# Performance work log

Hardware: AMD Instinct MI355X
Metric: run time of the kernel (lower is better)

The kernel has to match this reference:

```python
import jax, jax.numpy as jnp
import numpy as np

NUM_USERS = 40000
NUM_BUSINESSES = 60000
N = NUM_USERS + NUM_BUSINESSES
HIDDEN = 128
HEADS = 4
E = 200000
BATCH = 4096
NEG_SLOPE = 0.2  # PyG GATConv default


def setup_inputs() -> dict:
    key = jax.random.key(0)
    ks = jax.random.split(key, 20)
    s = 0.05
    inp = {
        "user_table": jax.random.normal(ks[0], (NUM_USERS, HIDDEN), jnp.float32) * s,
        "business_table": jax.random.normal(ks[1], (NUM_BUSINESSES, HIDDEN), jnp.float32) * s,
        # gat1: in=HIDDEN, out=HIDDEN, heads=HEADS
        "W1": jax.random.normal(ks[2], (HIDDEN, HEADS * HIDDEN), jnp.float32) * s,
        "att_src1": jax.random.normal(ks[3], (HEADS, HIDDEN), jnp.float32) * s,
        "att_dst1": jax.random.normal(ks[4], (HEADS, HIDDEN), jnp.float32) * s,
        "b1": jnp.zeros((HEADS * HIDDEN,), jnp.float32),
        # gat2: in=HEADS*HIDDEN, out=HIDDEN, heads=1
        "W2": jax.random.normal(ks[5], (HEADS * HIDDEN, HIDDEN), jnp.float32) * s,
        "att_src2": jax.random.normal(ks[6], (1, HIDDEN), jnp.float32) * s,
        "att_dst2": jax.random.normal(ks[7], (1, HIDDEN), jnp.float32) * s,
        "b2": jnp.zeros((HIDDEN,), jnp.float32),
        # predictor MLP
        "Wp1": jax.random.normal(ks[8], (2 * HIDDEN, HIDDEN), jnp.float32) * s,
        "bp1": jnp.zeros((HIDDEN,), jnp.float32),
        "Wp2": jax.random.normal(ks[9], (HIDDEN, 1), jnp.float32) * s,
        "bp2": jnp.zeros((1,), jnp.float32),
        "user_idx": jax.random.randint(ks[10], (BATCH,), 0, NUM_USERS),
        "business_idx": jax.random.randint(ks[11], (BATCH,), 0, NUM_BUSINESSES) + NUM_USERS,
        "edge_index": jax.random.randint(ks[12], (2, E), 0, N),
    }
    return inp


def gat_conv(x, edge_index, W, att_src, att_dst, bias, heads, out_ch, num_nodes):
    # add self-loops (PyG default add_self_loops=True)
    loop = jnp.arange(num_nodes)
    src = jnp.concatenate([edge_index[0], loop])
    dst = jnp.concatenate([edge_index[1], loop])
    h = (x @ W).reshape(num_nodes, heads, out_ch)            # [N,H,C]
    a_src = jnp.einsum('nhc,hc->nh', h, att_src)             # [N,H]
    a_dst = jnp.einsum('nhc,hc->nh', h, att_dst)             # [N,H]
    e = jax.nn.leaky_relu(a_src[src] + a_dst[dst], NEG_SLOPE)  # [E',H]
    # segment softmax over destination nodes
    emax = jax.ops.segment_max(e, dst, num_segments=num_nodes)
    emax = jnp.where(jnp.isfinite(emax), emax, 0.0)
    ex = jnp.exp(e - emax[dst])
    denom = jax.ops.segment_sum(ex, dst, num_segments=num_nodes)
    alpha = ex / (denom[dst] + 1e-16)                        # [E',H]
    msg = h[src] * alpha[..., None]                          # [E',H,C]
    out = jax.ops.segment_sum(msg, dst, num_segments=num_nodes)  # [N,H,C]
    return out.reshape(num_nodes, heads * out_ch) + bias


def reference(user_table, business_table, W1, att_src1, att_dst1, b1,
              W2, att_src2, att_dst2, b2, Wp1, bp1, Wp2, bp2,
              user_idx, business_idx, edge_index):
    user_emb = user_table[user_idx]                          # [B,HIDDEN]
    business_emb = business_table[business_idx - NUM_USERS]  # [B,HIDDEN]
    x = jnp.zeros((N, HIDDEN), jnp.float32)
    x = x.at[user_idx].set(user_emb)
    x = x.at[business_idx].set(business_emb)
    x = jax.nn.relu(gat_conv(x, edge_index, W1, att_src1, att_dst1, b1, HEADS, HIDDEN, N))
    x = gat_conv(x, edge_index, W2, att_src2, att_dst2, b2, 1, HIDDEN, N)
    feats = jnp.concatenate([x[user_idx], x[business_idx]], axis=1)  # [B,2*HIDDEN]
    hidden = jax.nn.relu(feats @ Wp1 + bp1)
    rating = hidden @ Wp2 + bp2                              # [B,1]
    return rating.squeeze(-1)
```

## Files before the change

kernel.cpp:

```cpp
#include <hip/hip_runtime.h>
#include <cstdint>
#include <cstddef>

#define NU      40000
#define NBZ     60000
#define NN      100000
#define HID     128
#define NHEADS  4
#define NE      200000
#define NBATCH  4096
#define BE      (2 * NBATCH)
#define SMAX    10240
#define CAP     16
#define SLOPE   0.2f

typedef __attribute__((ext_vector_type(8))) short short8v;
typedef __attribute__((ext_vector_type(4))) float f32x4;

__device__ __forceinline__ float lrelu(float x) { return x > 0.f ? x : SLOPE * x; }
__device__ __forceinline__ unsigned short f2bf(float f) {
  unsigned u = __float_as_uint(f);
  u += 0x7FFFu + ((u >> 16) & 1u);
  return (unsigned short)(u >> 16);
}

__global__ void k_init(int* __restrict__ node2slotB, int* __restrict__ flags,
                       int* __restrict__ cnt,
                       const float* __restrict__ W1, const float* __restrict__ W2,
                       const float* __restrict__ Wp1,
                       short* __restrict__ w1t, short* __restrict__ w2t,
                       short* __restrict__ wp1t) {
  int i = blockIdx.x * blockDim.x + threadIdx.x;
  if (i < NN) { node2slotB[i] = -1; flags[i] = 0; }
  if (i < NHEADS * HID * HID) {
    int c = i >> 14, nk = i & 16383, n = nk >> 7, k = nk & 127;
    w1t[i] = (short)f2bf(W1[(size_t)k * 512 + c * 128 + n]);
    w2t[i] = (short)f2bf(W2[(size_t)(c * 128 + k) * 128 + n]);
  }
  if (i < HID * 256) {
    int n = i >> 8, k = i & 255;
    wp1t[i] = (short)f2bf(Wp1[(size_t)k * HID + n]);
  }
  if (i == 0) *cnt = 0;
}

__global__ void k_mark(const int* __restrict__ user_idx, const int* __restrict__ business_idx,
                       int* __restrict__ node2slotB) {
  int i = blockIdx.x * blockDim.x + threadIdx.x;
  if (i >= BE) return;
  int node = (i < NBATCH) ? user_idx[i] : business_idx[i - NBATCH];
  node2slotB[node] = i;
}

#define W1ATT_BLOCKS 64
__global__ __launch_bounds__(256)
void k_frontA(const float* __restrict__ W1,
              const float* __restrict__ att_src1, const float* __restrict__ att_dst1,
              float* __restrict__ wsrc, float* __restrict__ wdst,
              const int* __restrict__ ei, const int* __restrict__ n2sB,
              int* __restrict__ flags) {
  int bid = blockIdx.x, tid = threadIdx.x;
  if (bid >= W1ATT_BLOCKS) {
    int e = (bid - W1ATT_BLOCKS) * 256 + tid;
    if (e < NE) {
      int s = ei[e], d = ei[NE + e];
      if (n2sB[d] >= 0) atomicOr(&flags[s], 2);
      if (n2sB[s] >= 0) atomicOr(&flags[d], 1);
    }
    return;
  }
  __shared__ float red[2][2][8];
  int kk = tid >> 7, c = tid & 127;
  int k = bid * 2 + kk;
  float ps[4], pd[4];
#pragma unroll
  for (int h = 0; h < 4; ++h) {
    float wv = W1[(size_t)k * 512 + h * 128 + c];
    ps[h] = wv * att_src1[h * 128 + c];
    pd[h] = wv * att_dst1[h * 128 + c];
  }
#pragma unroll
  for (int off = 1; off < 64; off <<= 1) {
#pragma unroll
    for (int h = 0; h < 4; ++h) { ps[h] += __shfl_xor(ps[h], off); pd[h] += __shfl_xor(pd[h], off); }
  }
  int half = (tid >> 6) & 1;
  if ((tid & 63) == 0) {
#pragma unroll
    for (int h = 0; h < 4; ++h) { red[kk][half][h] = ps[h]; red[kk][half][h + 4] = pd[h]; }
  }
  __syncthreads();
  if ((tid & 127) == 0) {
#pragma unroll
    for (int h = 0; h < 4; ++h) {
      wsrc[k * 4 + h] = red[kk][0][h] + red[kk][1][h];
      wdst[k * 4 + h] = red[kk][0][h + 4] + red[kk][1][h + 4];
    }
  }
}

#define SCAL1_BLOCKS (BE / 4)
__global__ __launch_bounds__(256)
void k_mid(const float* __restrict__ user_table, const float* __restrict__ business_table,
           const int* __restrict__ user_idx, const int* __restrict__ business_idx,
           const float* __restrict__ wsrc, const float* __restrict__ wdst,
           float* __restrict__ a_src1c, float* __restrict__ a_dst1c,
           const int* __restrict__ n2sB, const int* __restrict__ flags,
           int* __restrict__ slotN, int* __restrict__ slot2node, int* __restrict__ cnt,
           int* __restrict__ fillc1, int* __restrict__ indegS,
           int* __restrict__ fillc2, int* __restrict__ indegB) {
  int bid = blockIdx.x, tid = threadIdx.x;
  if (bid >= SCAL1_BLOCKS) {
    int v = (bid - SCAL1_BLOCKS) * 256 + tid;
    if (v >= NN) return;
    if (v < SMAX) { fillc1[v] = 0; indegS[v] = 0; }
    if (v < BE)   { fillc2[v] = 0; indegB[v] = 0; }
    bool need = (n2sB[v] >= 0) || ((flags[v] & 3) == 3);
    int s = -1;
    if (need) {
      s = atomicAdd(cnt, 1);
      if (s >= SMAX) s = -1;
      else slot2node[s] = v;
    }
    slotN[v] = s;
    return;
  }
  int w = bid * 4 + (tid >> 6);
  int lane = tid & 63;
  int node = (w < NBATCH) ? user_idx[w] : business_idx[w - NBATCH];
  const float* src = (w < NBATCH) ? (user_table + (size_t)node * HID)
                                  : (business_table + (size_t)(node - NU) * HID);
  float2 e = *(const float2*)(src + lane * 2);
  float4 w0s = *(const float4*)(wsrc + (lane * 2) * 4);
  float4 w1s = *(const float4*)(wsrc + (lane * 2 + 1) * 4);
  float4 w0d = *(const float4*)(wdst + (lane * 2) * 4);
  float4 w1d = *(const float4*)(wdst + (lane * 2 + 1) * 4);
  float ss[4] = {e.x * w0s.x + e.y * w1s.x, e.x * w0s.y + e.y * w1s.y,
                 e.x * w0s.z + e.y * w1s.z, e.x * w0s.w + e.y * w1s.w};
  float dd[4] = {e.x * w0d.x + e.y * w1d.x, e.x * w0d.y + e.y * w1d.y,
                 e.x * w0d.z + e.y * w1d.z, e.x * w0d.w + e.y * w1d.w};
#pragma unroll
  for (int off = 1; off < 64; off <<= 1) {
#pragma unroll
    for (int h = 0; h < 4; ++h) { ss[h] += __shfl_xor(ss[h], off); dd[h] += __shfl_xor(dd[h], off); }
  }
  if (lane == 0) {
    float4 o1 = {ss[0], ss[1], ss[2], ss[3]};
    float4 o2 = {dd[0], dd[1], dd[2], dd[3]};
    *(float4*)(a_src1c + w * 4) = o1;
    *(float4*)(a_dst1c + w * 4) = o2;
  }
}

__global__ void k_fillb(const int* __restrict__ ei, const int* __restrict__ n2sB,
                        const int* __restrict__ slotN,
                        int* __restrict__ fillc1, int* __restrict__ indegS, int* __restrict__ list1,
                        int* __restrict__ fillc2, int* __restrict__ indegB, int* __restrict__ list2) {
  int e = blockIdx.x * blockDim.x + threadIdx.x;
  if (e >= NE) return;
  int s = ei[e], d = ei[NE + e];
  int snd = slotN[d];
  if (snd >= 0) {
    atomicAdd(&indegS[snd], 1);
    int sB = n2sB[s];
    if (sB >= 0) { int p = atomicAdd(&fillc1[snd], 1); if (p < CAP) list1[snd * CAP + p] = sB; }
  }
  int dB = n2sB[d];
  if (dB >= 0) {
    atomicAdd(&indegB[dB], 1);
    int sns = slotN[s];
    if (sns >= 0) { int p = atomicAdd(&fillc2[dB], 1); if (p < CAP) list2[dB * CAP + p] = sns; }
  }
}

__global__ __launch_bounds__(256)
void k_agg1emb(const int* __restrict__ slot2node, const int* __restrict__ n2sB,
               const int* __restrict__ indegS, const int* __restrict__ fillc1,
               const int* __restrict__ list1,
               const float* __restrict__ a_src1c, const float* __restrict__ a_dst1c,
               const float* __restrict__ user_table, const float* __restrict__ business_table,
               const int* __restrict__ user_idx, const int* __restrict__ business_idx,
               const int* __restrict__ cntp, short* __restrict__ eaggb) {
  int w = (blockIdx.x * blockDim.x + threadIdx.x) >> 6;
  int lane = threadIdx.x & 63;
  int M = *cntp; if (M > SMAX) M = SMAX;
  if (w >= M) return;
  int v = slot2node[w];
  int dB = n2sB[v];
  float ad[4] = {0.f, 0.f, 0.f, 0.f};
  if (dB >= 0) {
    float4 a = *(const float4*)(a_dst1c + dB * 4);
    ad[0] = a.x; ad[1] = a.y; ad[2] = a.z; ad[3] = a.w;
  }
  int ne = fillc1[w];
  int nnb = indegS[w] + 1 - ne - (dB >= 0 ? 1 : 0);
  float m[4], sum[4], ax[4], ay[4];
#pragma unroll
  for (int h = 0; h < 4; ++h) {
    if (nnb > 0) { m[h] = lrelu(ad[h]); sum[h] = (float)nnb; }
    else { m[h] = -3.0e38f; sum[h] = 0.f; }
    ax[h] = 0.f; ay[h] = 0.f;
  }
  for (int j = (dB >= 0 ? -1 : 0); j < ne; ++j) {
    int sB = (j < 0) ? dB : list1[w * CAP + j];
    float4 as4 = *(const float4*)(a_src1c + sB * 4);
    float as[4] = {as4.x, as4.y, as4.z, as4.w};
    int node = (sB < NBATCH) ? user_idx[sB] : business_idx[sB - NBATCH];
    const float* src = (sB < NBATCH) ? (user_table + (size_t)node * HID)
                                     : (business_table + (size_t)(node - NU) * HID);
    float2 e = *(const float2*)(src + lane * 2);
#pragma unroll
    for (int h = 0; h < 4; ++h) {
      float x = lrelu(as[h] + ad[h]);
      if (x > m[h]) {
        float r = __expf(m[h] - x);
        sum[h] = sum[h] * r + 1.f;
        ax[h] = ax[h] * r + e.x;
        ay[h] = ay[h] * r + e.y;
        m[h] = x;
      } else {
        float p = __expf(x - m[h]);
        sum[h] += p;
        ax[h] += p * e.x;
        ay[h] += p * e.y;
      }
    }
  }
  unsigned short* o = (unsigned short*)eaggb + (size_t)w * 512;
#pragma unroll
  for (int h = 0; h < 4; ++h) {
    float r = 1.f / (sum[h] + 1e-16f);
    unsigned lo = f2bf(ax[h] * r), hi = f2bf(ay[h] * r);
    *(unsigned*)(o + h * 128 + lane * 2) = lo | (hi << 16);
  }
}

__global__ __launch_bounds__(256)
void k_mm0(const short* __restrict__ A, const short* __restrict__ Bt,
           const float* __restrict__ bias, const int* __restrict__ cntp,
           short* __restrict__ T) {
  int M = *cntp; if (M > SMAX) M = SMAX;
  int row0 = blockIdx.x * 64;
  if (row0 >= M) return;
  int c = blockIdx.y;
  int lane = threadIdx.x & 63;
  int wid = threadIdx.x >> 6;
  int l15 = lane & 15, g = lane >> 4;
  int kq = g * 8;
  f32x4 acc[4][2];
#pragma unroll
  for (int i = 0; i < 4; ++i)
#pragma unroll
    for (int j = 0; j < 2; ++j) acc[i][j] = (f32x4){0.f, 0.f, 0.f, 0.f};

#pragma unroll
  for (int k0 = 0; k0 < 128; k0 += 32) {
    short8v av[4], bv[2];
#pragma unroll
    for (int i = 0; i < 4; ++i) {
      int rA = row0 + i * 16 + l15; if (rA >= M) rA = M - 1;
      av[i] = *(const short8v*)(A + (size_t)rA * 512 + c * 128 + k0 + kq);
    }
#pragma unroll
    for (int j = 0; j < 2; ++j) {
      int col = wid * 32 + j * 16 + l15;
      bv[j] = *(const short8v*)(Bt + ((size_t)c * 128 + col) * 128 + k0 + kq);
    }
#pragma unroll
    for (int i = 0; i < 4; ++i)
#pragma unroll
      for (int j = 0; j < 2; ++j)
        acc[i][j] = __builtin_amdgcn_mfma_f32_16x16x32_bf16(av[i], bv[j], acc[i][j], 0, 0, 0);
  }
#pragma unroll
  for (int j = 0; j < 2; ++j) {
    int col = wid * 32 + j * 16 + l15;
    float bvv = bias[c * 128 + col];
#pragma unroll
    for (int i = 0; i < 4; ++i) {
#pragma unroll
      for (int q = 0; q < 4; ++q) {
        int r = row0 + i * 16 + g * 4 + q;
        if (r < M)
          ((unsigned short*)T)[(size_t)r * 512 + c * 128 + col] = f2bf(fmaxf(acc[i][j][q] + bvv, 0.f));
      }
    }
  }
}

__global__ __launch_bounds__(256)
void k_mm1p(const short* __restrict__ T, const short* __restrict__ Bt,
            const int* __restrict__ cntp, float* __restrict__ part) {
  int M = *cntp; if (M > SMAX) M = SMAX;
  int row0 = blockIdx.x * 64;
  if (row0 >= M) return;
  int c = blockIdx.z;
  int lane = threadIdx.x & 63;
  int wid = threadIdx.x >> 6;
  int l15 = lane & 15, g = lane >> 4;
  int kq = g * 8;
  f32x4 acc[4][2];
#pragma unroll
  for (int i = 0; i < 4; ++i)
#pragma unroll
    for (int j = 0; j < 2; ++j) acc[i][j] = (f32x4){0.f, 0.f, 0.f, 0.f};

#pragma unroll
  for (int k0 = 0; k0 < 128; k0 += 32) {
    short8v av[4], bv[2];
#pragma unroll
    for (int i = 0; i < 4; ++i) {
      int rA = row0 + i * 16 + l15; if (rA >= M) rA = M - 1;
      av[i] = *(const short8v*)(T + (size_t)rA * 512 + c * 128 + k0 + kq);
    }
#pragma unroll
    for (int j = 0; j < 2; ++j) {
      int col = wid * 32 + j * 16 + l15;
      bv[j] = *(const short8v*)(Bt + ((size_t)c * 128 + col) * 128 + k0 + kq);
    }
#pragma unroll
    for (int i = 0; i < 4; ++i)
#pragma unroll
      for (int j = 0; j < 2; ++j)
        acc[i][j] = __builtin_amdgcn_mfma_f32_16x16x32_bf16(av[i], bv[j], acc[i][j], 0, 0, 0);
  }
  float* Cp = part + (size_t)c * SMAX * HID;
#pragma unroll
  for (int j = 0; j < 2; ++j) {
    int col = wid * 32 + j * 16 + l15;
#pragma unroll
    for (int i = 0; i < 4; ++i) {
#pragma unroll
      for (int q = 0; q < 4; ++q) {
        int r = row0 + i * 16 + g * 4 + q;
        if (r < M) Cp[(size_t)r * HID + col] = acc[i][j][q];
      }
    }
  }
}

__global__ void k_h2red(const float* __restrict__ part,
                        const float* __restrict__ att_src2, const float* __restrict__ att_dst2,
                        float* __restrict__ h2c, float* __restrict__ a_src2c,
                        float* __restrict__ a_dst2c, const int* __restrict__ cnt) {
  int w = (blockIdx.x * blockDim.x + threadIdx.x) >> 6;
  int lane = threadIdx.x & 63;
  int M = *cnt; if (M > SMAX) M = SMAX;
  if (w >= M) return;
  int c = lane * 2;
  size_t off = (size_t)w * HID + c;
  float2 p0 = *(const float2*)(part + off);
  float2 p1 = *(const float2*)(part + (size_t)SMAX * HID + off);
  float2 p2 = *(const float2*)(part + (size_t)2 * SMAX * HID + off);
  float2 p3 = *(const float2*)(part + (size_t)3 * SMAX * HID + off);
  float h0 = p0.x + p1.x + p2.x + p3.x;
  float h1 = p0.y + p1.y + p2.y + p3.y;
  float2 o = {h0, h1};
  *(float2*)(h2c + off) = o;
  float ss = h0 * att_src2[c] + h1 * att_src2[c + 1];
  float dd = h0 * att_dst2[c] + h1 * att_dst2[c + 1];
  for (int off2 = 1; off2 < 64; off2 <<= 1) { ss += __shfl_xor(ss, off2); dd += __shfl_xor(dd, off2); }
  if (lane == 0) { a_src2c[w] = ss; a_dst2c[w] = dd; }
}

__global__ __launch_bounds__(256)
void k_agg2(const int* __restrict__ user_idx, const int* __restrict__ business_idx,
            const int* __restrict__ n2sB, const int* __restrict__ slotN,
            const int* __restrict__ indegB, const int* __restrict__ fillc2,
            const int* __restrict__ list2,
            const float* __restrict__ a_src2c, const float* __restrict__ a_dst2c,
            const float* __restrict__ h2c, const float* __restrict__ b2,
            short* __restrict__ x2b) {
  int w = (blockIdx.x * blockDim.x + threadIdx.x) >> 6;
  int lane = threadIdx.x & 63;
  if (w >= BE) return;
  int node = (w < NBATCH) ? user_idx[w] : business_idx[w - NBATCH];
  if (n2sB[node] != w) return;
  int snd = slotN[node];
  float ad = a_dst2c[snd];
  int ne = fillc2[w];
  int nnb = indegB[w] - ne;
  float m, sum;
  if (nnb > 0) { m = lrelu(ad); sum = (float)nnb; } else { m = -3.0e38f; sum = 0.f; }
  float a0 = 0.f, a1 = 0.f;
  for (int j = -1; j < ne; ++j) {
    int sn = (j < 0) ? snd : list2[w * CAP + j];
    float x = lrelu(a_src2c[sn] + ad);
    float2 hv = *(const float2*)(h2c + (size_t)sn * HID + lane * 2);
    if (x > m) {
      float r = __expf(m - x);
      sum = sum * r + 1.f;
      a0 = a0 * r + hv.x;
      a1 = a1 * r + hv.y;
      m = x;
    } else {
      float p = __expf(x - m);
      sum += p;
      a0 += p * hv.x;
      a1 += p * hv.y;
    }
  }
  float r = 1.f / (sum + 1e-16f);
  int c0 = lane * 2;
  unsigned lo = f2bf(a0 * r + b2[c0]);
  unsigned hi = f2bf(a1 * r + b2[c0 + 1]);
  *(unsigned*)((unsigned short*)x2b + (size_t)w * HID + c0) = lo | (hi << 16);
}

__global__ __launch_bounds__(512)
void k_mlp(const short* __restrict__ x2b, const short* __restrict__ wp1t,
           const int* __restrict__ user_idx, const int* __restrict__ business_idx,
           const int* __restrict__ n2sB,
           const float* __restrict__ bp1, const float* __restrict__ Wp2,
           const float* __restrict__ bp2, float* __restrict__ out) {
  __shared__ float pout[8][16];
  int row0 = blockIdx.x * 16;
  int lane = threadIdx.x & 63;
  int w = threadIdx.x >> 6;
  int l15 = lane & 15, g = lane >> 4;
  int kq = g * 8;
  int p = row0 + l15;
  int us = n2sB[user_idx[p]];
  int bs = n2sB[business_idx[p]];
  int nn = w * 16 + l15;
  f32x4 acc = {0.f, 0.f, 0.f, 0.f};
  const short* bpw = wp1t + (size_t)nn * 256 + kq;
#pragma unroll
  for (int k0 = 0; k0 < 256; k0 += 32) {
    int slot = (k0 < 128) ? us : bs;
    short8v a = *(const short8v*)(x2b + (size_t)slot * HID + (k0 & 127) + kq);
    short8v b = *(const short8v*)(bpw + k0);
    acc = __builtin_amdgcn_mfma_f32_16x16x32_bf16(a, b, acc, 0, 0, 0);
  }
  float bpv = bp1[nn], wpv = Wp2[nn];
#pragma unroll
  for (int j = 0; j < 4; ++j) {
    float v = fmaxf(acc[j] + bpv, 0.f) * wpv;
#pragma unroll
    for (int off = 1; off < 16; off <<= 1) v += __shfl_xor(v, off);
    if (l15 == 0) pout[w][g * 4 + j] = v;
  }
  __syncthreads();
  int tid = threadIdx.x;
  if (tid < 16) {
    float s = 0.f;
#pragma unroll
    for (int q = 0; q < 8; ++q) s += pout[q][tid];
    out[row0 + tid] = s + bp2[0];
  }
}

extern "C" void kernel_launch(void* const* d_in, const int* in_sizes, int n_in,
                              void* d_out, int out_size, void* d_ws, size_t ws_size,
                              hipStream_t stream) {
  const float* user_table     = (const float*)d_in[0];
  const float* business_table = (const float*)d_in[1];
  const float* W1       = (const float*)d_in[2];
  const float* att_src1 = (const float*)d_in[3];
  const float* att_dst1 = (const float*)d_in[4];
  const float* b1       = (const float*)d_in[5];
  const float* W2       = (const float*)d_in[6];
  const float* att_src2 = (const float*)d_in[7];
  const float* att_dst2 = (const float*)d_in[8];
  const float* b2       = (const float*)d_in[9];
  const float* Wp1      = (const float*)d_in[10];
  const float* bp1      = (const float*)d_in[11];
  const float* Wp2      = (const float*)d_in[12];
  const float* bp2      = (const float*)d_in[13];
  const int* user_idx     = (const int*)d_in[14];
  const int* business_idx = (const int*)d_in[15];
  const int* ei           = (const int*)d_in[16];
  float* out = (float*)d_out;

  char* w = (char*)d_ws;
  size_t used = 0;
  auto alloc = [&](size_t bytes) -> void* {
    void* p = w + used;
    used += (bytes + 255) & ~(size_t)255;
    return p;
  };
  int*   node2slotB = (int*)alloc((size_t)NN * 4);
  int*   flags      = (int*)alloc((size_t)NN * 4);
  int*   slotN      = (int*)alloc((size_t)NN * 4);
  int*   slot2node  = (int*)alloc((size_t)SMAX * 4);
  int*   cnt        = (int*)alloc(256);
  float* wsrc       = (float*)alloc((size_t)HID * 4 * 4);
  float* wdst       = (float*)alloc((size_t)HID * 4 * 4);
  float* a_src1c    = (float*)alloc((size_t)BE * 4 * 4);
  float* a_dst1c    = (float*)alloc((size_t)BE * 4 * 4);
  int*   fillc1     = (int*)alloc((size_t)SMAX * 4);
  int*   indegS     = (int*)alloc((size_t)SMAX * 4);
  int*   list1      = (int*)alloc((size_t)SMAX * CAP * 4);
  int*   fillc2     = (int*)alloc((size_t)BE * 4);
  int*   indegB     = (int*)alloc((size_t)BE * 4);
  int*   list2      = (int*)alloc((size_t)BE * CAP * 4);
  short* w1t        = (short*)alloc((size_t)NHEADS * HID * HID * 2);
  short* w2t        = (short*)alloc((size_t)NHEADS * HID * HID * 2);
  short* wp1t       = (short*)alloc((size_t)HID * 256 * 2);
  short* eaggb      = (short*)alloc((size_t)SMAX * 512 * 2);
  short* tbufb      = (short*)alloc((size_t)SMAX * 512 * 2);
  float* part       = (float*)alloc((size_t)4 * SMAX * HID * 4);
  float* h2c        = (float*)alloc((size_t)SMAX * HID * 4);
  float* a_src2c    = (float*)alloc((size_t)SMAX * 4);
  float* a_dst2c    = (float*)alloc((size_t)SMAX * 4);
  short* x2b        = (short*)alloc((size_t)BE * HID * 2);
  if (used > ws_size) return;

  const int T = 256;
  auto cdiv = [](int a, int b) { return (a + b - 1) / b; };

  k_init<<<cdiv(NN, T), T, 0, stream>>>(node2slotB, flags, cnt, W1, W2, Wp1, w1t, w2t, wp1t);
  k_mark<<<cdiv(BE, T), T, 0, stream>>>(user_idx, business_idx, node2slotB);

  k_frontA<<<W1ATT_BLOCKS + cdiv(NE, T), T, 0, stream>>>(
      W1, att_src1, att_dst1, wsrc, wdst, ei, node2slotB, flags);

  k_mid<<<SCAL1_BLOCKS + cdiv(NN, T), T, 0, stream>>>(
      user_table, business_table, user_idx, business_idx, wsrc, wdst,
      a_src1c, a_dst1c, node2slotB, flags, slotN, slot2node, cnt,
      fillc1, indegS, fillc2, indegB);

  k_fillb<<<cdiv(NE, T), T, 0, stream>>>(ei, node2slotB, slotN,
                                         fillc1, indegS, list1, fillc2, indegB, list2);

  k_agg1emb<<<cdiv(SMAX * 64, T), T, 0, stream>>>(
      slot2node, node2slotB, indegS, fillc1, list1, a_src1c, a_dst1c,
      user_table, business_table, user_idx, business_idx, cnt, eaggb);

  k_mm0<<<dim3(SMAX / 64, NHEADS), T, 0, stream>>>(eaggb, w1t, b1, cnt, tbufb);
  k_mm1p<<<dim3(SMAX / 64, 1, NHEADS), T, 0, stream>>>(tbufb, w2t, cnt, part);
  k_h2red<<<cdiv(SMAX * 64, T), T, 0, stream>>>(part, att_src2, att_dst2,
                                                h2c, a_src2c, a_dst2c, cnt);

  k_agg2<<<cdiv(BE * 64, T), T, 0, stream>>>(user_idx, business_idx, node2slotB, slotN,
                                             indegB, fillc2, list2, a_src2c, a_dst2c,
                                             h2c, b2, x2b);

  k_mlp<<<NBATCH / 16, 512, 0, stream>>>(x2b, wp1t, user_idx, business_idx, node2slotB,
                                         bp1, Wp2, bp2, out);
}
```

Measured before the change: 99.46 us.

## Fuse h2 reduction into agg2, move weight transposes into frontA, memset init

Removes the k_h2red kernel. k_agg2h now sums the four partial matmul outputs and computes the layer-2 attention scores on the fly for each neighbor it visits, so the h2c and a_src2c/a_dst2c buffers go away. The bf16 weight transposes move out of k_init into extra blocks of k_frontA, and node2slotB/flags are cleared with hipMemsetAsync using a +1 offset encoding so that zero means unmapped. The aim is fewer launches and less intermediate memory traffic. The cost is redundant partial-sum reads and extra shuffle reductions per neighbor in agg2.

```diff
diff --git a/kernel.cpp b/kernel.cpp
--- a/kernel.cpp
+++ b/kernel.cpp
@@ -24,48 +24,49 @@
   return (unsigned short)(u >> 16);
 }
 
-__global__ void k_init(int* __restrict__ node2slotB, int* __restrict__ flags,
-                       int* __restrict__ cnt,
-                       const float* __restrict__ W1, const float* __restrict__ W2,
-                       const float* __restrict__ Wp1,
-                       short* __restrict__ w1t, short* __restrict__ w2t,
-                       short* __restrict__ wp1t) {
+
+__global__ void k_mark(const int* __restrict__ user_idx, const int* __restrict__ business_idx,
+                       int* __restrict__ node2slotB, int* __restrict__ cnt) {
   int i = blockIdx.x * blockDim.x + threadIdx.x;
-  if (i < NN) { node2slotB[i] = -1; flags[i] = 0; }
-  if (i < NHEADS * HID * HID) {
-    int c = i >> 14, nk = i & 16383, n = nk >> 7, k = nk & 127;
-    w1t[i] = (short)f2bf(W1[(size_t)k * 512 + c * 128 + n]);
-    w2t[i] = (short)f2bf(W2[(size_t)(c * 128 + k) * 128 + n]);
-  }
-  if (i < HID * 256) {
-    int n = i >> 8, k = i & 255;
-    wp1t[i] = (short)f2bf(Wp1[(size_t)k * HID + n]);
-  }
   if (i == 0) *cnt = 0;
-}
-
-__global__ void k_mark(const int* __restrict__ user_idx, const int* __restrict__ business_idx,
-                       int* __restrict__ node2slotB) {
-  int i = blockIdx.x * blockDim.x + threadIdx.x;
   if (i >= BE) return;
   int node = (i < NBATCH) ? user_idx[i] : business_idx[i - NBATCH];
-  node2slotB[node] = i;
+  node2slotB[node] = i + 1;
 }
 
 #define W1ATT_BLOCKS 64
+#define WT_BLOCKS    640
 __global__ __launch_bounds__(256)
-void k_frontA(const float* __restrict__ W1,
+void k_frontA(const float* __restrict__ W1, const float* __restrict__ W2,
+              const float* __restrict__ Wp1,
               const float* __restrict__ att_src1, const float* __restrict__ att_dst1,
               float* __restrict__ wsrc, float* __restrict__ wdst,
+              short* __restrict__ w1t, short* __restrict__ w2t, short* __restrict__ wp1t,
               const int* __restrict__ ei, const int* __restrict__ n2sB,
               int* __restrict__ flags) {
   int bid = blockIdx.x, tid = threadIdx.x;
-  if (bid >= W1ATT_BLOCKS) {
-    int e = (bid - W1ATT_BLOCKS) * 256 + tid;
+  if (bid >= W1ATT_BLOCKS + WT_BLOCKS) {
+    int e = (bid - W1ATT_BLOCKS - WT_BLOCKS) * 256 + tid;
     if (e < NE) {
       int s = ei[e], d = ei[NE + e];
-      if (n2sB[d] >= 0) atomicOr(&flags[s], 2);
-      if (n2sB[s] >= 0) atomicOr(&flags[d], 1);
+      if (n2sB[d] > 0) atomicOr(&flags[s], 2);
+      if (n2sB[s] > 0) atomicOr(&flags[d], 1);
+    }
+    return;
+  }
+  if (bid >= W1ATT_BLOCKS) {
+    int t = (bid - W1ATT_BLOCKS) * 256 + tid;
+    if (t < 65536) {
+      int c = t >> 14, kn = t & 16383, k = kn >> 7, n = kn & 127;
+      w1t[c * 16384 + n * 128 + k] = (short)f2bf(W1[(size_t)k * 512 + c * 128 + n]);
+    } else if (t < 131072) {
+      int t2 = t - 65536;
+      int c = t2 >> 14, kn = t2 & 16383, k = kn >> 7, n = kn & 127;
+      w2t[c * 16384 + n * 128 + k] = (short)f2bf(W2[(size_t)(c * 128 + k) * 128 + n]);
+    } else if (t < 163840) {
+      int t3 = t - 131072;
+      int k = t3 >> 7, n = t3 & 127;
+      wp1t[n * 256 + k] = (short)f2bf(Wp1[(size_t)k * HID + n]);
     }
     return;
   }
@@ -115,7 +116,7 @@
     if (v >= NN) return;
     if (v < SMAX) { fillc1[v] = 0; indegS[v] = 0; }
     if (v < BE)   { fillc2[v] = 0; indegB[v] = 0; }
-    bool need = (n2sB[v] >= 0) || ((flags[v] & 3) == 3);
+    bool need = (n2sB[v] > 0) || ((flags[v] & 3) == 3);
     int s = -1;
     if (need) {
       s = atomicAdd(cnt, 1);
@@ -162,11 +163,12 @@
   int snd = slotN[d];
   if (snd >= 0) {
     atomicAdd(&indegS[snd], 1);
-    int sB = n2sB[s];
-    if (sB >= 0) { int p = atomicAdd(&fillc1[snd], 1); if (p < CAP) list1[snd * CAP + p] = sB; }
-  }
-  int dB = n2sB[d];
-  if (dB >= 0) {
+    int sBr = n2sB[s];
+    if (sBr > 0) { int p = atomicAdd(&fillc1[snd], 1); if (p < CAP) list1[snd * CAP + p] = sBr - 1; }
+  }
+  int dBr = n2sB[d];
+  if (dBr > 0) {
+    int dB = dBr - 1;
     atomicAdd(&indegB[dB], 1);
     int sns = slotN[s];
     if (sns >= 0) { int p = atomicAdd(&fillc2[dB], 1); if (p < CAP) list2[dB * CAP + p] = sns; }
@@ -186,7 +188,7 @@
   int M = *cntp; if (M > SMAX) M = SMAX;
   if (w >= M) return;
   int v = slot2node[w];
-  int dB = n2sB[v];
+  int dB = n2sB[v] - 1;
   float ad[4] = {0.f, 0.f, 0.f, 0.f};
   if (dB >= 0) {
     float4 a = *(const float4*)(a_dst1c + dB * 4);
@@ -339,69 +341,61 @@
   }
 }
 
-__global__ void k_h2red(const float* __restrict__ part,
-                        const float* __restrict__ att_src2, const float* __restrict__ att_dst2,
-                        float* __restrict__ h2c, float* __restrict__ a_src2c,
-                        float* __restrict__ a_dst2c, const int* __restrict__ cnt) {
-  int w = (blockIdx.x * blockDim.x + threadIdx.x) >> 6;
-  int lane = threadIdx.x & 63;
-  int M = *cnt; if (M > SMAX) M = SMAX;
-  if (w >= M) return;
-  int c = lane * 2;
-  size_t off = (size_t)w * HID + c;
-  float2 p0 = *(const float2*)(part + off);
-  float2 p1 = *(const float2*)(part + (size_t)SMAX * HID + off);
-  float2 p2 = *(const float2*)(part + (size_t)2 * SMAX * HID + off);
-  float2 p3 = *(const float2*)(part + (size_t)3 * SMAX * HID + off);
-  float h0 = p0.x + p1.x + p2.x + p3.x;
-  float h1 = p0.y + p1.y + p2.y + p3.y;
-  float2 o = {h0, h1};
-  *(float2*)(h2c + off) = o;
-  float ss = h0 * att_src2[c] + h1 * att_src2[c + 1];
-  float dd = h0 * att_dst2[c] + h1 * att_dst2[c + 1];
-  for (int off2 = 1; off2 < 64; off2 <<= 1) { ss += __shfl_xor(ss, off2); dd += __shfl_xor(dd, off2); }
-  if (lane == 0) { a_src2c[w] = ss; a_dst2c[w] = dd; }
-}
-
 __global__ __launch_bounds__(256)
-void k_agg2(const int* __restrict__ user_idx, const int* __restrict__ business_idx,
-            const int* __restrict__ n2sB, const int* __restrict__ slotN,
-            const int* __restrict__ indegB, const int* __restrict__ fillc2,
-            const int* __restrict__ list2,
-            const float* __restrict__ a_src2c, const float* __restrict__ a_dst2c,
-            const float* __restrict__ h2c, const float* __restrict__ b2,
-            short* __restrict__ x2b) {
+void k_agg2h(const int* __restrict__ user_idx, const int* __restrict__ business_idx,
+             const int* __restrict__ n2sB, const int* __restrict__ slotN,
+             const int* __restrict__ indegB, const int* __restrict__ fillc2,
+             const int* __restrict__ list2, const float* __restrict__ part,
+             const float* __restrict__ att_src2, const float* __restrict__ att_dst2,
+             const float* __restrict__ b2, short* __restrict__ x2b) {
   int w = (blockIdx.x * blockDim.x + threadIdx.x) >> 6;
   int lane = threadIdx.x & 63;
   if (w >= BE) return;
   int node = (w < NBATCH) ? user_idx[w] : business_idx[w - NBATCH];
-  if (n2sB[node] != w) return;
+  if (n2sB[node] != w + 1) return;
   int snd = slotN[node];
-  float ad = a_dst2c[snd];
+  int c0 = lane * 2;
+  float as2a = att_src2[c0], as2b = att_src2[c0 + 1];
+  float ad2a = att_dst2[c0], ad2b = att_dst2[c0 + 1];
+  size_t offS = (size_t)snd * HID + c0;
+  float2 q0 = *(const float2*)(part + offS);
+  float2 q1 = *(const float2*)(part + (size_t)SMAX * HID + offS);
+  float2 q2 = *(const float2*)(part + (size_t)2 * SMAX * HID + offS);
+  float2 q3 = *(const float2*)(part + (size_t)3 * SMAX * HID + offS);
+  float hs0 = q0.x + q1.x + q2.x + q3.x;
+  float hs1 = q0.y + q1.y + q2.y + q3.y;
+  float ssS = hs0 * as2a + hs1 * as2b;
+  float adS = hs0 * ad2a + hs1 * ad2b;
+#pragma unroll
+  for (int off = 1; off < 64; off <<= 1) { ssS += __shfl_xor(ssS, off); adS += __shfl_xor(adS, off); }
+  float ad = adS;
   int ne = fillc2[w];
   int nnb = indegB[w] - ne;
   float m, sum;
   if (nnb > 0) { m = lrelu(ad); sum = (float)nnb; } else { m = -3.0e38f; sum = 0.f; }
   float a0 = 0.f, a1 = 0.f;
-  for (int j = -1; j < ne; ++j) {
-    int sn = (j < 0) ? snd : list2[w * CAP + j];
-    float x = lrelu(a_src2c[sn] + ad);
-    float2 hv = *(const float2*)(h2c + (size_t)sn * HID + lane * 2);
-    if (x > m) {
-      float r = __expf(m - x);
-      sum = sum * r + 1.f;
-      a0 = a0 * r + hv.x;
-      a1 = a1 * r + hv.y;
-      m = x;
-    } else {
-      float p = __expf(x - m);
-      sum += p;
-      a0 += p * hv.x;
-      a1 += p * hv.y;
-    }
+  {
+    float x = lrelu(ssS + ad);
+    if (x > m) { float r = __expf(m - x); sum = sum * r + 1.f; a0 = a0 * r + hs0; a1 = a1 * r + hs1; m = x; }
+    else { float p = __expf(x - m); sum += p; a0 += p * hs0; a1 += p * hs1; }
+  }
+  for (int j = 0; j < ne; ++j) {
+    int sn = list2[w * CAP + j];
+    size_t off2 = (size_t)sn * HID + c0;
+    float2 p0 = *(const float2*)(part + off2);
+    float2 p1 = *(const float2*)(part + (size_t)SMAX * HID + off2);
+    float2 p2 = *(const float2*)(part + (size_t)2 * SMAX * HID + off2);
+    float2 p3 = *(const float2*)(part + (size_t)3 * SMAX * HID + off2);
+    float r0 = p0.x + p1.x + p2.x + p3.x;
+    float r1 = p0.y + p1.y + p2.y + p3.y;
+    float ss = r0 * as2a + r1 * as2b;
+#pragma unroll
+    for (int off = 1; off < 64; off <<= 1) ss += __shfl_xor(ss, off);
+    float x = lrelu(ss + ad);
+    if (x > m) { float r = __expf(m - x); sum = sum * r + 1.f; a0 = a0 * r + r0; a1 = a1 * r + r1; m = x; }
+    else { float p = __expf(x - m); sum += p; a0 += p * r0; a1 += p * r1; }
   }
   float r = 1.f / (sum + 1e-16f);
-  int c0 = lane * 2;
   unsigned lo = f2bf(a0 * r + b2[c0]);
   unsigned hi = f2bf(a1 * r + b2[c0 + 1]);
   *(unsigned*)((unsigned short*)x2b + (size_t)w * HID + c0) = lo | (hi << 16);
@@ -420,8 +414,8 @@
   int l15 = lane & 15, g = lane >> 4;
   int kq = g * 8;
   int p = row0 + l15;
-  int us = n2sB[user_idx[p]];
-  int bs = n2sB[business_idx[p]];
+  int us = n2sB[user_idx[p]] - 1;
+  int bs = n2sB[business_idx[p]] - 1;
   int nn = w * 16 + l15;
   f32x4 acc = {0.f, 0.f, 0.f, 0.f};
   const short* bpw = wp1t + (size_t)nn * 256 + kq;
@@ -500,20 +494,20 @@
   short* eaggb      = (short*)alloc((size_t)SMAX * 512 * 2);
   short* tbufb      = (short*)alloc((size_t)SMAX * 512 * 2);
   float* part       = (float*)alloc((size_t)4 * SMAX * HID * 4);
-  float* h2c        = (float*)alloc((size_t)SMAX * HID * 4);
-  float* a_src2c    = (float*)alloc((size_t)SMAX * 4);
-  float* a_dst2c    = (float*)alloc((size_t)SMAX * 4);
   short* x2b        = (short*)alloc((size_t)BE * HID * 2);
   if (used > ws_size) return;
 
   const int T = 256;
   auto cdiv = [](int a, int b) { return (a + b - 1) / b; };
 
-  k_init<<<cdiv(NN, T), T, 0, stream>>>(node2slotB, flags, cnt, W1, W2, Wp1, w1t, w2t, wp1t);
-  k_mark<<<cdiv(BE, T), T, 0, stream>>>(user_idx, business_idx, node2slotB);
-
-  k_frontA<<<W1ATT_BLOCKS + cdiv(NE, T), T, 0, stream>>>(
-      W1, att_src1, att_dst1, wsrc, wdst, ei, node2slotB, flags);
+  hipMemsetAsync(node2slotB, 0, (size_t)NN * 4, stream);
+  hipMemsetAsync(flags, 0, (size_t)NN * 4, stream);
+
+  k_mark<<<cdiv(BE, T), T, 0, stream>>>(user_idx, business_idx, node2slotB, cnt);
+
+  k_frontA<<<W1ATT_BLOCKS + WT_BLOCKS + cdiv(NE, T), T, 0, stream>>>(
+      W1, W2, Wp1, att_src1, att_dst1, wsrc, wdst, w1t, w2t, wp1t,
+      ei, node2slotB, flags);
 
   k_mid<<<SCAL1_BLOCKS + cdiv(NN, T), T, 0, stream>>>(
       user_table, business_table, user_idx, business_idx, wsrc, wdst,
@@ -529,12 +523,10 @@
 
   k_mm0<<<dim3(SMAX / 64, NHEADS), T, 0, stream>>>(eaggb, w1t, b1, cnt, tbufb);
   k_mm1p<<<dim3(SMAX / 64, 1, NHEADS), T, 0, stream>>>(tbufb, w2t, cnt, part);
-  k_h2red<<<cdiv(SMAX * 64, T), T, 0, stream>>>(part, att_src2, att_dst2,
-                                                h2c, a_src2c, a_dst2c, cnt);
-
-  k_agg2<<<cdiv(BE * 64, T), T, 0, stream>>>(user_idx, business_idx, node2slotB, slotN,
-                                             indegB, fillc2, list2, a_src2c, a_dst2c,
-                                             h2c, b2, x2b);
+
+  k_agg2h<<<cdiv(BE * 64, T), T, 0, stream>>>(user_idx, business_idx, node2slotB, slotN,
+                                              indegB, fillc2, list2, part,
+                                              att_src2, att_dst2, b2, x2b);
 
   k_mlp<<<NBATCH / 16, 512, 0, stream>>>(x2b, wp1t, user_idx, business_idx, node2slotB,
                                          bp1, Wp2, bp2, out);
```

Result: no change. 100.4 us (+0.9%).
